# Kernel optimization log

Measured on AMD Instinct MI355X. Metric: run time of the kernel, lower is better.

The kernel has to match this reference:

```python
import jax, jax.numpy as jnp
import numpy as np

N_COARSE = 64
N_FINE = 128
MIN_DEPTH = 2.0
MAX_DEPTH = 6.0
B = 131072


def setup_inputs() -> dict:
    key = jax.random.key(0)
    k1, k2, k3, k4, k5 = jax.random.split(key, 5)
    origins = jax.random.normal(k1, (B, 3), dtype=jnp.float32)
    directions = jax.random.normal(k2, (B, 3), dtype=jnp.float32)
    density = jax.random.uniform(k3, (B, N_COARSE, 1), dtype=jnp.float32)
    t_rand = jax.random.uniform(k4, (B, N_COARSE), dtype=jnp.float32)
    u = jax.random.uniform(k5, (B, N_FINE), dtype=jnp.float32)
    return {"origins": origins, "directions": directions, "density": density,
            "t_rand": t_rand, "u": u}


def _forward(origins, directions, density, t_rand, u):
    b = origins.shape[0]
    # ---- coarse stratified sampling (training branch) ----
    z = jnp.broadcast_to(jnp.linspace(MIN_DEPTH, MAX_DEPTH, N_COARSE, dtype=jnp.float32), (b, N_COARSE))
    mids = 0.5 * (z[..., 1:] + z[..., :-1])
    upper = jnp.concatenate([mids, z[..., -1:]], axis=-1)
    lower = jnp.concatenate([z[..., :1], mids], axis=-1)
    z_vals = lower + (upper - lower) * t_rand  # [B, Nc]
    coarse_points = origins[:, None, :] + directions[:, None, :] * z_vals[..., None]  # [B, Nc, 3]

    # ---- transmittance weights (no_grad in original) ----
    deltas = jnp.concatenate([z_vals[..., 1:] - z_vals[..., :-1],
                              jnp.full((b, 1), 1e10, dtype=z_vals.dtype)], axis=-1)  # [B, Nc]
    alpha = 1.0 - jnp.exp(-density[..., 0] * deltas)  # [B, Nc]
    # exclusive cumulative product: T_i = prod_{j<i} (1 - alpha_j + 1e-10)
    T = jnp.concatenate([jnp.ones((b, 1), dtype=alpha.dtype),
                         jnp.cumprod(1.0 - alpha + 1e-10, axis=-1)[..., :-1]], axis=-1)
    weights = jax.lax.stop_gradient(alpha * T)  # [B, Nc]

    # ---- inverse-CDF fine sampling ----
    w = weights + 1e-5
    pdf = w / jnp.sum(w, axis=-1, keepdims=True)
    cdf = jnp.concatenate([jnp.zeros((b, 1), dtype=pdf.dtype), jnp.cumsum(pdf, axis=-1)], axis=-1)  # [B, Nc+1]

    z_edges = 0.5 * (z_vals[..., 1:] + z_vals[..., :-1])
    z_edges = jnp.concatenate([
        z_vals[..., :1] - 0.5 * (z_vals[..., 1:2] - z_vals[..., :1]),
        z_edges,
        z_vals[..., -1:] + 0.5 * (z_vals[..., -1:] - z_vals[..., -2:-1])], axis=-1)  # [B, Nc+1]

    inds = jax.vmap(lambda c, uu: jnp.searchsorted(c, uu, side='right'))(cdf, u)  # [B, Nf]
    below = jnp.clip(inds - 1, 0, cdf.shape[-1] - 1)
    above = jnp.clip(inds, 0, cdf.shape[-1] - 1)

    cdf_g0 = jnp.take_along_axis(cdf, below, axis=-1)
    cdf_g1 = jnp.take_along_axis(cdf, above, axis=-1)
    e0 = jnp.take_along_axis(z_edges, below, axis=-1)
    e1 = jnp.take_along_axis(z_edges, above, axis=-1)

    denom = cdf_g1 - cdf_g0
    denom = jnp.where(denom < 1e-5, jnp.ones_like(denom), denom)
    t = (u - cdf_g0) / denom
    fine_z = e0 + t * (e1 - e0)  # [B, Nf]
    fine_points = origins[:, None, :] + directions[:, None, :] * fine_z[..., None]  # [B, Nf, 3]

    # ---- merge + sort along depth ----
    all_points = jnp.concatenate([coarse_points, fine_points], axis=1)  # [B, Nc+Nf, 3]
    all_z = jnp.concatenate([z_vals, fine_z], axis=1)                   # [B, Nc+Nf]
    idx = jnp.argsort(all_z, axis=-1)
    all_z = jnp.take_along_axis(all_z, idx, axis=-1)
    all_points = jnp.take_along_axis(all_points, idx[..., None], axis=1)
    return all_points, all_z


def reference(origins, directions, density, t_rand, u):
    return _forward(origins, directions, density, t_rand, u)
```

## Files before the change

### kernel.cpp

```cpp
#include <hip/hip_runtime.h>

#define RPW 4
#define RPB 8
#define RSTR 324

typedef float vf4 __attribute__((ext_vector_type(4)));

template<int CTRL, bool BC>
__device__ __forceinline__ float updpp(float old, float x) {
    return __int_as_float(__builtin_amdgcn_update_dpp(
        __float_as_int(old), __float_as_int(x), CTRL, 0xF, 0xF, BC));
}

template<int K, int J>
__device__ __forceinline__ void substage(float (&y)[16], const int sl) {
    if constexpr (J >= 16) {
        constexpr int lm = J >> 4;
        const bool uasc = ((sl & (K >> 4)) == 0);
        const bool lo4  = ((sl & 4) == 0);
        #pragma unroll
        for (int h = 0; h < 16; ++h) {
            float p;
            if constexpr (lm == 1)      p = updpp<0xB1, true>(0.0f, y[h]);
            else if constexpr (lm == 2) p = updpp<0x4E, true>(0.0f, y[h]);
            else if constexpr (lm == 8) p = updpp<0x128,true>(0.0f, y[h]);
            else {
                float r4  = updpp<0x124,true>(0.0f, y[h]);
                float r12 = updpp<0x12C,true>(0.0f, y[h]);
                p = lo4 ? r12 : r4;
            }
            const bool tmin = (((sl & lm) == 0) == uasc);
            y[h] = tmin ? fminf(y[h], p) : fmaxf(y[h], p);
        }
    } else {
        bool dirlane = true;
        if constexpr (K == 16)      dirlane = ((sl & 1) == 0);
        else if constexpr (K >= 32) dirlane = ((sl & (K >> 4)) == 0);
        #pragma unroll
        for (int h = 0; h < 16; ++h) {
            if ((h & J) == 0) {
                const int b = h ^ J;
                bool dr;
                if constexpr (K <= 8) dr = ((h & K) == 0);
                else                  dr = dirlane;
                float lo_ = fminf(y[h], y[b]);
                float hi_ = fmaxf(y[h], y[b]);
                y[h] = dr ? lo_ : hi_;
                y[b] = dr ? hi_ : lo_;
            }
        }
    }
}

__global__ __launch_bounds__(128) void hier_sampler(
    const float* __restrict__ org, const float* __restrict__ dir,
    const float* __restrict__ dens, const float* __restrict__ trand,
    const float* __restrict__ uu, float* __restrict__ out_pts,
    float* __restrict__ out_z)
{
    const int tid  = threadIdx.x;
    const int sl   = tid & 15;
    const int rloc = tid >> 4;
    const int ray  = blockIdx.x * RPB + rloc;

    __shared__ __align__(16) float lds[RPB * RSTR];
    float* srt  = &lds[rloc * RSTR];
    float* cdfB = srt + 192;
    float* edg  = srt + 256;

    const float4 t4 = ((const float4*)trand)[(size_t)ray * 16 + sl];
    const float4 d4 = ((const float4*)dens )[(size_t)ray * 16 + sl];
    const float4 ua = ((const float4*)uu)[(size_t)ray*32 + 2*sl];
    const float4 ub = ((const float4*)uu)[(size_t)ray*32 + 2*sl + 1];
    const float ox = org[(size_t)ray*3+0], oy = org[(size_t)ray*3+1], oz = org[(size_t)ray*3+2];
    const float dx = dir[(size_t)ray*3+0], dy = dir[(size_t)ray*3+1], dz = dir[(size_t)ray*3+2];

    const float step = 4.0f / 63.0f;
    const float tarr[4] = {t4.x, t4.y, t4.z, t4.w};
    const float darr[4] = {d4.x, d4.y, d4.z, d4.w};
    float zv[4];
    #pragma unroll
    for (int m = 0; m < 4; ++m) {
        int j = 4*sl + m;
        float zg = 2.0f + step * (float)j;
        float lo = (j == 0)  ? 2.0f : (zg - 0.5f*step);
        float up = (j == 63) ? 6.0f : (zg + 0.5f*step);
        zv[m] = lo + (up - lo) * tarr[m];
    }
    float znext0 = updpp<0x101,true>(0.0f, zv[0]);
    float delta[4] = { zv[1]-zv[0], zv[2]-zv[1], zv[3]-zv[2],
                       (sl == 15) ? 1e10f : (znext0 - zv[3]) };

    float a[4], pp[4];
    {
        float run = 1.0f;
        #pragma unroll
        for (int m = 0; m < 4; ++m) {
            a[m] = 1.0f - __expf(-darr[m] * delta[m]);
            run *= (1.0f - a[m] + 1e-10f);
            pp[m] = run;
        }
    }
    float P = pp[3];
    P *= updpp<0x111,false>(1.0f, P);
    P *= updpp<0x112,false>(1.0f, P);
    P *= updpp<0x114,false>(1.0f, P);
    P *= updpp<0x118,false>(1.0f, P);
    float E = updpp<0x111,false>(1.0f, P);

    float sw[4];
    {
        float acc = 0.0f;
        #pragma unroll
        for (int m = 0; m < 4; ++m) {
            float T = (m == 0) ? E : E * pp[m-1];
            acc += a[m]*T + 1e-5f;
            sw[m] = acc;
        }
    }
    float S = sw[3];
    S += updpp<0x111,false>(0.0f, S);
    S += updpp<0x112,false>(0.0f, S);
    S += updpp<0x114,false>(0.0f, S);
    S += updpp<0x118,false>(0.0f, S);
    float Es  = updpp<0x111,false>(0.0f, S);
    float tot = __shfl(S, 15, 16);
    float itot = 1.0f / tot;

    *(float4*)(cdfB + 4*sl) = make_float4((Es+sw[0])*itot, (Es+sw[1])*itot,
                                          (Es+sw[2])*itot, (Es+sw[3])*itot);
    float bb  = Es + sw[0];
    float c16 = __shfl(bb, 4, 16)  * itot;
    float c32 = __shfl(bb, 8, 16)  * itot;
    float c48 = __shfl(bb, 12, 16) * itot;

    float zp3 = updpp<0x111,true>(0.0f, zv[3]);
    float ej0 = (sl == 0) ? (1.5f*zv[0] - 0.5f*zv[1]) : 0.5f*(zp3 + zv[0]);
    *(float4*)(edg + 4*sl) = make_float4(ej0, 0.5f*(zv[0]+zv[1]),
                                         0.5f*(zv[1]+zv[2]), 0.5f*(zv[2]+zv[3]));
    if (sl == 15) edg[64] = 1.5f*zv[3] - 0.5f*zv[2];
    *(float4*)(srt + 4*sl) = make_float4(zv[0], zv[1], zv[2], zv[3]);

    const float uarr[8] = {ua.x,ua.y,ua.z,ua.w, ub.x,ub.y,ub.z,ub.w};
    float fz[8];
    #pragma unroll
    for (int t = 0; t < 8; ++t) {
        float u = uarr[t];
        bool d0 = (c32 <= u);
        int  lo = d0 ? 33 : 0;
        int  hi = d0 ? 64 : 32;
        float cm1 = d0 ? c48 : c16;
        int  m1 = (lo + hi) >> 1;
        bool d1 = (cm1 <= u);
        lo = d1 ? m1 + 1 : lo;
        hi = d1 ? hi : m1;
        #pragma unroll
        for (int it = 0; it < 5; ++it) {
            int m = (lo + hi) >> 1;
            bool c = cdfB[m] <= u;
            lo = c ? m+1 : lo;
            hi = c ? hi  : m;
        }
        int below = lo;
        int above = (lo < 64) ? lo + 1 : 64;
        int bm1   = (below > 0) ? below - 1 : 0;
        float c0 = cdfB[bm1];
        if (below == 0) c0 = 0.0f;
        float c1 = cdfB[above - 1];
        float e0 = edg[below], e1 = edg[above];
        float dn = c1 - c0;
        if (dn < 1e-5f) dn = 1.0f;
        float tt = (u - c0) / dn;
        fz[t] = e0 + tt * (e1 - e0);
    }
    *(float4*)(srt + 64 + 8*sl)     = make_float4(fz[0],fz[1],fz[2],fz[3]);
    *(float4*)(srt + 64 + 8*sl + 4) = make_float4(fz[4],fz[5],fz[6],fz[7]);

    float y[16];
    if (sl < 12) {
        #pragma unroll
        for (int tq = 0; tq < 4; ++tq) {
            float4 v = *(const float4*)(srt + 16*sl + 4*tq);
            y[4*tq+0]=v.x; y[4*tq+1]=v.y; y[4*tq+2]=v.z; y[4*tq+3]=v.w;
        }
    } else {
        #pragma unroll
        for (int h = 0; h < 16; ++h) y[h] = 1.0e30f;
    }

    substage<2,1>(y, sl);

    substage<4,2>(y, sl);   substage<4,1>(y, sl);

    substage<8,4>(y, sl);   substage<8,2>(y, sl);   substage<8,1>(y, sl);

    substage<16,8>(y, sl);  substage<16,4>(y, sl);  substage<16,2>(y, sl);
    substage<16,1>(y, sl);

    substage<32,16>(y, sl); substage<32,8>(y, sl);  substage<32,4>(y, sl);
    substage<32,2>(y, sl);  substage<32,1>(y, sl);

    substage<64,32>(y, sl); substage<64,16>(y, sl); substage<64,8>(y, sl);
    substage<64,4>(y, sl);  substage<64,2>(y, sl);  substage<64,1>(y, sl);

    substage<128,64>(y, sl); substage<128,32>(y, sl); substage<128,16>(y, sl);
    substage<128,8>(y, sl);  substage<128,4>(y, sl);  substage<128,2>(y, sl);
    substage<128,1>(y, sl);

    substage<256,128>(y, sl); substage<256,64>(y, sl); substage<256,32>(y, sl);
    substage<256,16>(y, sl);  substage<256,8>(y, sl);  substage<256,4>(y, sl);
    substage<256,2>(y, sl);   substage<256,1>(y, sl);

    if (sl < 12) {
        #pragma unroll
        for (int tq = 0; tq < 4; ++tq) {
            *(float4*)(srt + 16*sl + 4*tq) =
                make_float4(y[4*tq],y[4*tq+1],y[4*tq+2],y[4*tq+3]);
        }
    }

    {
        float* zb = out_z + (size_t)ray * 192;
        #pragma unroll
        for (int it = 0; it < 3; ++it) {
            int c = it * 16 + sl;
            vf4 v = *(const vf4*)(srt + 4*c);
            __builtin_nontemporal_store(v, (vf4*)(zb + 4*c));
        }
    }

    float* pbase = out_pts + (size_t)ray * 576;
    #pragma unroll
    for (int it = 0; it < 9; ++it) {
        int i  = it*16 + sl;
        int q  = i / 3;
        int c0 = i - 3*q;
        int k0 = i + q;
        const float* zp = srt + k0;
        float z0 = zp[0];
        float z1 = zp[1];
        float o0  = (c0==0)?ox:((c0==1)?oy:oz);
        float dd0 = (c0==0)?dx:((c0==1)?dy:dz);
        float v0 = fmaf(dd0, z0, o0);
        float v3 = fmaf(dd0, z1, o0);
        int   c1i = (c0==2)?0:(c0+1);
        float zz1 = (c0==2)?z1:z0;
        float o1  = (c1i==0)?ox:((c1i==1)?oy:oz);
        float dd1 = (c1i==0)?dx:((c1i==1)?dy:dz);
        float v1 = fmaf(dd1, zz1, o1);
        int   c2i = (c0==0)?2:(c0-1);
        float zz2 = (c0==0)?z0:z1;
        float o2  = (c2i==0)?ox:((c2i==1)?oy:oz);
        float dd2 = (c2i==0)?dx:((c2i==1)?dy:dz);
        float v2 = fmaf(dd2, zz2, o2);
        vf4 v = {v0, v1, v2, v3};
        __builtin_nontemporal_store(v, (vf4*)(pbase + 4*i));
    }
}

extern "C" void kernel_launch(void* const* d_in, const int* in_sizes, int n_in,
                              void* d_out, int out_size, void* d_ws, size_t ws_size,
                              hipStream_t stream) {
    const float* org   = (const float*)d_in[0];
    const float* dir   = (const float*)d_in[1];
    const float* dens  = (const float*)d_in[2];
    const float* trand = (const float*)d_in[3];
    const float* uv    = (const float*)d_in[4];
    int B = in_sizes[0] / 3;

    float* out_pts = (float*)d_out;
    float* out_z   = out_pts + (size_t)B * 576;

    dim3 grid(B / RPB), block(128);
    hipLaunchKernelGGL(hier_sampler, grid, block, 0, stream,
                       org, dir, dens, trand, uv, out_pts, out_z);
}
```

Before: 138.9 us.

## Exploit sorted coarse samples: sort fine samples only, then bitonic merge

The full 256-element bitonic sort of the combined coarse and fine depths is replaced. The 128 fine samples are bitonic-sorted in registers, 8 per lane, with descending order chosen so that, concatenated with the already-sorted coarse samples, they form a bitonic sequence. A single merge pass (8 substages) then finishes the sort. Padding becomes -1e30 in the low lanes, and the store offset shifts by four lanes. This removes most compare-exchange and DPP work but relies on the coarse z_vals already being ascending.

Measured after the change: 118.6 us. 14.6% less time.

```diff
diff --git a/kernel.cpp b/kernel.cpp
--- a/kernel.cpp
+++ b/kernel.cpp
@@ -12,41 +12,67 @@
         __float_as_int(old), __float_as_int(x), CTRL, 0xF, 0xF, BC));
 }
 
+template<int LM>
+__device__ __forceinline__ float xl(float x, const bool lo4) {
+    if constexpr (LM == 1)      return updpp<0xB1, true>(0.0f, x);
+    else if constexpr (LM == 2) return updpp<0x4E, true>(0.0f, x);
+    else if constexpr (LM == 8) return updpp<0x128,true>(0.0f, x);
+    else {
+        float r4  = updpp<0x124,true>(0.0f, x);
+        float r12 = updpp<0x12C,true>(0.0f, x);
+        return lo4 ? r12 : r4;
+    }
+}
+
+#define CE(a, b, dir) { float _lo = fminf(a, b), _hi = fmaxf(a, b); \
+                        a = (dir) ? _lo : _hi; b = (dir) ? _hi : _lo; }
+
 template<int K, int J>
-__device__ __forceinline__ void substage(float (&y)[16], const int sl) {
+__device__ __forceinline__ void substageF(float (&f)[8], const int sl) {
+    if constexpr (J >= 8) {
+        constexpr int lm = J >> 3;
+        const bool uasc = ((sl & (K >> 3)) != 0);
+        const bool lo4  = ((sl & 4) == 0);
+        #pragma unroll
+        for (int h = 0; h < 8; ++h) {
+            float p = xl<lm>(f[h], lo4);
+            const bool tmin = (uasc == ((sl & lm) == 0));
+            f[h] = tmin ? fminf(f[h], p) : fmaxf(f[h], p);
+        }
+    } else {
+        bool dirlane = true;
+        if constexpr (K == 8)       dirlane = ((sl & 1) != 0);
+        else if constexpr (K >= 16) dirlane = ((sl & (K >> 3)) != 0);
+        #pragma unroll
+        for (int h = 0; h < 8; ++h) {
+            if ((h & J) == 0) {
+                const int b = h ^ J;
+                bool dr;
+                if constexpr (K <= 4) dr = ((h & K) != 0);
+                else                  dr = dirlane;
+                CE(f[h], f[b], dr);
+            }
+        }
+    }
+}
+
+template<int J>
+__device__ __forceinline__ void substageM(float (&y)[16], const int sl) {
     if constexpr (J >= 16) {
         constexpr int lm = J >> 4;
-        const bool uasc = ((sl & (K >> 4)) == 0);
-        const bool lo4  = ((sl & 4) == 0);
+        const bool lo4 = ((sl & 4) == 0);
         #pragma unroll
         for (int h = 0; h < 16; ++h) {
-            float p;
-            if constexpr (lm == 1)      p = updpp<0xB1, true>(0.0f, y[h]);
-            else if constexpr (lm == 2) p = updpp<0x4E, true>(0.0f, y[h]);
-            else if constexpr (lm == 8) p = updpp<0x128,true>(0.0f, y[h]);
-            else {
-                float r4  = updpp<0x124,true>(0.0f, y[h]);
-                float r12 = updpp<0x12C,true>(0.0f, y[h]);
-                p = lo4 ? r12 : r4;
-            }
-            const bool tmin = (((sl & lm) == 0) == uasc);
+            float p = xl<lm>(y[h], lo4);
+            const bool tmin = ((sl & lm) == 0);
             y[h] = tmin ? fminf(y[h], p) : fmaxf(y[h], p);
         }
     } else {
-        bool dirlane = true;
-        if constexpr (K == 16)      dirlane = ((sl & 1) == 0);
-        else if constexpr (K >= 32) dirlane = ((sl & (K >> 4)) == 0);
         #pragma unroll
         for (int h = 0; h < 16; ++h) {
             if ((h & J) == 0) {
                 const int b = h ^ J;
-                bool dr;
-                if constexpr (K <= 8) dr = ((h & K) == 0);
-                else                  dr = dirlane;
-                float lo_ = fminf(y[h], y[b]);
-                float hi_ = fmaxf(y[h], y[b]);
-                y[h] = dr ? lo_ : hi_;
-                y[b] = dr ? hi_ : lo_;
+                CE(y[h], y[b], true);
             }
         }
     }
@@ -173,6 +199,20 @@
         float tt = (u - c0) / dn;
         fz[t] = e0 + tt * (e1 - e0);
     }
+
+    substageF<2,1>(fz, sl);
+    substageF<4,2>(fz, sl);    substageF<4,1>(fz, sl);
+    substageF<8,4>(fz, sl);    substageF<8,2>(fz, sl);    substageF<8,1>(fz, sl);
+    substageF<16,8>(fz, sl);   substageF<16,4>(fz, sl);   substageF<16,2>(fz, sl);
+    substageF<16,1>(fz, sl);
+    substageF<32,16>(fz, sl);  substageF<32,8>(fz, sl);   substageF<32,4>(fz, sl);
+    substageF<32,2>(fz, sl);   substageF<32,1>(fz, sl);
+    substageF<64,32>(fz, sl);  substageF<64,16>(fz, sl);  substageF<64,8>(fz, sl);
+    substageF<64,4>(fz, sl);   substageF<64,2>(fz, sl);   substageF<64,1>(fz, sl);
+    substageF<128,64>(fz, sl); substageF<128,32>(fz, sl); substageF<128,16>(fz, sl);
+    substageF<128,8>(fz, sl);  substageF<128,4>(fz, sl);  substageF<128,2>(fz, sl);
+    substageF<128,1>(fz, sl);
+
     *(float4*)(srt + 64 + 8*sl)     = make_float4(fz[0],fz[1],fz[2],fz[3]);
     *(float4*)(srt + 64 + 8*sl + 4) = make_float4(fz[4],fz[5],fz[6],fz[7]);
 
@@ -185,36 +225,17 @@
         }
     } else {
         #pragma unroll
-        for (int h = 0; h < 16; ++h) y[h] = 1.0e30f;
-    }
-
-    substage<2,1>(y, sl);
-
-    substage<4,2>(y, sl);   substage<4,1>(y, sl);
-
-    substage<8,4>(y, sl);   substage<8,2>(y, sl);   substage<8,1>(y, sl);
-
-    substage<16,8>(y, sl);  substage<16,4>(y, sl);  substage<16,2>(y, sl);
-    substage<16,1>(y, sl);
-
-    substage<32,16>(y, sl); substage<32,8>(y, sl);  substage<32,4>(y, sl);
-    substage<32,2>(y, sl);  substage<32,1>(y, sl);
-
-    substage<64,32>(y, sl); substage<64,16>(y, sl); substage<64,8>(y, sl);
-    substage<64,4>(y, sl);  substage<64,2>(y, sl);  substage<64,1>(y, sl);
-
-    substage<128,64>(y, sl); substage<128,32>(y, sl); substage<128,16>(y, sl);
-    substage<128,8>(y, sl);  substage<128,4>(y, sl);  substage<128,2>(y, sl);
-    substage<128,1>(y, sl);
-
-    substage<256,128>(y, sl); substage<256,64>(y, sl); substage<256,32>(y, sl);
-    substage<256,16>(y, sl);  substage<256,8>(y, sl);  substage<256,4>(y, sl);
-    substage<256,2>(y, sl);   substage<256,1>(y, sl);
-
-    if (sl < 12) {
+        for (int h = 0; h < 16; ++h) y[h] = -1.0e30f;
+    }
+
+    substageM<128>(y, sl); substageM<64>(y, sl); substageM<32>(y, sl);
+    substageM<16>(y, sl);  substageM<8>(y, sl);  substageM<4>(y, sl);
+    substageM<2>(y, sl);   substageM<1>(y, sl);
+
+    if (sl >= 4) {
         #pragma unroll
         for (int tq = 0; tq < 4; ++tq) {
-            *(float4*)(srt + 16*sl + 4*tq) =
+            *(float4*)(srt + 16*(sl-4) + 4*tq) =
                 make_float4(y[4*tq],y[4*tq+1],y[4*tq+2],y[4*tq+3]);
         }
     }
```
